# Kernel tuning notes

Hardware: AMD Instinct MI355X
Metric: run time of the kernel (lower is better)

Reference implementation:

```python
import jax, jax.numpy as jnp
import numpy as np

EMBED_DIM = 1024
NUM_HEADS = 16
HEAD_DIM = EMBED_DIM // NUM_HEADS


def setup_inputs() -> dict:
    key = jax.random.key(0)
    ks = jax.random.split(key, 5)
    T, B, E = 2048, 2, EMBED_DIM
    s = 1.0 / np.sqrt(E)
    return {
        "x": jax.random.normal(ks[0], (T, B, E), jnp.float32),
        "wq": jax.random.normal(ks[1], (E, E), jnp.float32) * s,
        "bq": jnp.zeros((E,), jnp.float32),
        "wk": jax.random.normal(ks[2], (E, E), jnp.float32) * s,
        "bk": jnp.zeros((E,), jnp.float32),
        "wv": jax.random.normal(ks[3], (E, E), jnp.float32) * s,
        "bv": jnp.zeros((E,), jnp.float32),
        "wo": jax.random.normal(ks[4], (E, E), jnp.float32) * s,
        "bo": jnp.zeros((E,), jnp.float32),
    }


def reference(x, wq, bq, wk, bk, wv, bv, wo, bo):
    # x: [T, B, E] (Time x Batch x Channel), self-attention: query = key = value = x
    T, B, E = x.shape
    H, D = NUM_HEADS, HEAD_DIM
    scaling = D ** -0.5
    # Linear projections (torch Linear: y = x @ W.T + b)
    q = (jnp.einsum('tbe,fe->tbf', x, wq) + bq) * scaling
    k = jnp.einsum('tbe,fe->tbf', x, wk) + bk
    v = jnp.einsum('tbe,fe->tbf', x, wv) + bv
    # reshape to [B*H, T, D] equivalent -> use [B, H, T, D]
    q = q.reshape(T, B, H, D).transpose(1, 2, 0, 3)  # [B,H,T,D]
    k = k.reshape(T, B, H, D).transpose(1, 2, 0, 3)
    v = v.reshape(T, B, H, D).transpose(1, 2, 0, 3)
    # scores: [B,H,T,S], fp32 softmax
    scores = jnp.einsum('bhtd,bhsd->bhts', q, k)
    probs = jax.nn.softmax(scores.astype(jnp.float32), axis=-1).astype(x.dtype)
    attn = jnp.einsum('bhts,bhsd->bhtd', probs, v)  # [B,H,T,D]
    attn = attn.transpose(2, 0, 1, 3).reshape(T, B, E)
    out = jnp.einsum('tbe,fe->tbf', attn, wo) + bo
    return out
```

## Files before the change

kernel.cpp:

```cpp
#include <hip/hip_runtime.h>
#include <cstddef>
#include <cstdint>

#define T_DIM 2048
#define E_DIM 1024
#define M_DIM 4096

typedef __attribute__((ext_vector_type(8))) short short8;
typedef __attribute__((ext_vector_type(8))) _Float16 half8;
typedef __attribute__((ext_vector_type(4))) _Float16 half4;
typedef __attribute__((ext_vector_type(4))) float f32x4;

__device__ __forceinline__ short f16_bits(float v) {
  return __builtin_bit_cast(short, (_Float16)v);
}
__device__ __forceinline__ unsigned int pk2(float a, float b) {
  return __builtin_bit_cast(unsigned int, __builtin_amdgcn_cvt_pkrtz(a, b));
}
__device__ __forceinline__ half8 h8(short8 s) { return __builtin_bit_cast(half8, s); }

__device__ __forceinline__ void gl_lds16(const short* g, const short* l) {
  __builtin_amdgcn_global_load_lds(
      (const __attribute__((address_space(1))) unsigned int*)g,
      (__attribute__((address_space(3))) unsigned int*)l, 16, 0, 0);
}

__global__ __launch_bounds__(256) void convert_all(
    const float* __restrict__ x, const float* __restrict__ wq,
    const float* __restrict__ wk, const float* __restrict__ wv,
    const float* __restrict__ wo,
    short* __restrict__ xh, short* __restrict__ wqh, short* __restrict__ wkh,
    short* __restrict__ wvh, short* __restrict__ woh)
{
  const int bid = blockIdx.x;
  const float* in; short* hi; int base;
  if (bid < 4096)      { in = x;  hi = xh;  base = 0;    }
  else if (bid < 5120) { in = wq; hi = wqh; base = 4096; }
  else if (bid < 6144) { in = wk; hi = wkh; base = 5120; }
  else if (bid < 7168) { in = wv; hi = wvh; base = 6144; }
  else                 { in = wo; hi = woh; base = 7168; }
  const int i = (bid - base) * 256 + threadIdx.x;
  float4 v = ((const float4*)in)[i];
  uint2 p;
  p.x = (unsigned short)f16_bits(v.x) | ((unsigned int)(unsigned short)f16_bits(v.y) << 16);
  p.y = (unsigned short)f16_bits(v.z) | ((unsigned int)(unsigned short)f16_bits(v.w) << 16);
  ((uint2*)hi)[i] = p;
}

__global__ __launch_bounds__(256) void gemm_qkv(
    const short* __restrict__ xh,
    const short* __restrict__ wqh, const short* __restrict__ wkh,
    const short* __restrict__ wvh,
    const float* __restrict__ bq, const float* __restrict__ bk,
    const float* __restrict__ bv,
    short* __restrict__ qo, short* __restrict__ ko, short* __restrict__ vto)
{
  __shared__ __align__(16) short smem[128 * 64 * 2];
  short* Ah = smem;
  short* Wh = smem + 8192;
  const int tid = threadIdx.x;
  const int lane = tid & 63;
  const int w = tid >> 6;
  const int quad = lane >> 4;
  const int l15 = lane & 15;
  const int sel = blockIdx.x >> 3;
  const int n0 = (blockIdx.x & 7) * 128;
  const int m0 = blockIdx.y * 128;

  const short* wsel = sel == 0 ? wqh : sel == 1 ? wkh : wvh;
  const float* bias = sel == 0 ? bq : sel == 1 ? bk : bv;
  const float scale = sel == 0 ? 0.125f * 1.44269504088896f : 1.0f;

  const short* gsrc = (w < 2) ? xh : wsel;
  short* lbuf = (w < 2) ? Ah : Wh;
  const int rbase = (w < 2) ? m0 : n0;
  const int lrow8 = lane >> 3;
  const int gph8 = lane & 7;
  const int kg = (gph8 - lrow8) & 7;

  f32x4 zero = {0.f, 0.f, 0.f, 0.f};
  f32x4 acc[4][4];
#pragma unroll
  for (int i = 0; i < 4; ++i)
#pragma unroll
    for (int j = 0; j < 4; ++j) acc[i][j] = zero;

  const int wm = w & 1, wn = w >> 1;

  for (int k0 = 0; k0 < E_DIM; k0 += 64) {
    __syncthreads();
#pragma unroll
    for (int jj = 0; jj < 8; ++jj) {
      int j = (w & 1) * 8 + jj;
      int r = j * 8 + lrow8;
      gl_lds16(gsrc + (size_t)(rbase + r) * E_DIM + k0 + kg * 8, lbuf + j * 512);
    }
    __syncthreads();
#pragma unroll
    for (int ks = 0; ks < 2; ++ks) {
      short8 ahf[4];
#pragma unroll
      for (int i = 0; i < 4; ++i) {
        int r = wm * 64 + i * 16 + l15;
        ahf[i] = *(const short8*)&Ah[r * 64 + ((ks * 4 + quad + r) & 7) * 8];
      }
#pragma unroll
      for (int j = 0; j < 4; ++j) {
        int r = wn * 64 + j * 16 + l15;
        short8 bhf = *(const short8*)&Wh[r * 64 + ((ks * 4 + quad + r) & 7) * 8];
#pragma unroll
        for (int i = 0; i < 4; ++i)
          acc[i][j] = __builtin_amdgcn_mfma_f32_16x16x32_f16(h8(ahf[i]), h8(bhf), acc[i][j], 0, 0, 0);
      }
    }
  }

  if (sel < 2) {
#pragma unroll
    for (int j = 0; j < 4; ++j) {
      const int gc = n0 + wn * 64 + j * 16 + l15;
      const float bb = bias[gc];
      const int h = gc >> 6, d = gc & 63;
      short* dst = sel == 0 ? qo : ko;
#pragma unroll
      for (int i = 0; i < 4; ++i)
#pragma unroll
        for (int reg = 0; reg < 4; ++reg) {
          const int gm = m0 + wm * 64 + i * 16 + quad * 4 + reg;
          const float val = (acc[i][j][reg] + bb) * scale;
          const int t = gm >> 1, b = gm & 1;
          dst[((size_t)(b * 16 + h) * T_DIM + t) * 64 + d] = f16_bits(val);
        }
    }
  } else {
    short* Tb = smem;
    const int by = blockIdx.y;
#pragma unroll
    for (int R = 0; R < 2; ++R) {
      __syncthreads();
      if (wn == R) {
#pragma unroll
        for (int j = 0; j < 4; ++j) {
          const int nl = j * 16 + l15;
          const int gc = n0 + R * 64 + nl;
          const float bb = bias[gc];
#pragma unroll
          for (int i = 0; i < 4; ++i) {
            const int tp = wm * 32 + i * 8 + quad * 2;
            unsigned int lo = pk2(acc[i][j][0] + bb, acc[i][j][2] + bb);
            unsigned int hi = pk2(acc[i][j][1] + bb, acc[i][j][3] + bb);
            const int g0 = tp >> 3;
            const int sub = tp & 7;
            *(unsigned int*)&Tb[nl * 128 + ((g0 + nl) & 15) * 8 + sub] = lo;
            *(unsigned int*)&Tb[nl * 128 + ((g0 + 8 + nl) & 15) * 8 + sub] = hi;
          }
        }
      }
      __syncthreads();
#pragma unroll
      for (int ii = 0; ii < 4; ++ii) {
        const int n = w * 16 + ii * 4 + quad;
        const int g = (l15 - n) & 15;
        short8 vvec = *(const short8*)&Tb[n * 128 + l15 * 8];
        const int gc = n0 + R * 64 + n;
        const int h = gc >> 6, d = gc & 63;
        const int b = g >> 3;
        const int t = by * 64 + (g & 7) * 8;
        *(short8*)&vto[((size_t)(b * 16 + h) * 64 + d) * T_DIM + t] = vvec;
      }
    }
  }
}

__global__ __launch_bounds__(512, 4) void gemm_out_fused(
    const short* __restrict__ attn, const short* __restrict__ woh,
    const float* __restrict__ bo, float* __restrict__ out)
{
  __shared__ __align__(16) short smem[32768];
  const int tid = threadIdx.x;
  const int lane = tid & 63;
  const int w = tid >> 6;
  const int g = w >> 2;
  const int wg = w & 3;
  const int quad = lane >> 4;
  const int l15 = lane & 15;
  const int n0 = blockIdx.x * 128;
  const int m0 = blockIdx.y * 128;

  short* Ah = smem + g * 16384;
  short* Wh = Ah + 8192;
  const short* gsrc = (wg < 2) ? attn : woh;
  short* lbuf = (wg < 2) ? Ah : Wh;
  const int rbase = (wg < 2) ? m0 : n0;
  const int lrow8 = lane >> 3;
  const int gph8 = lane & 7;
  const int kg = (gph8 - lrow8) & 7;

  f32x4 zero = {0.f, 0.f, 0.f, 0.f};
  f32x4 acc[4][4];
#pragma unroll
  for (int i = 0; i < 4; ++i)
#pragma unroll
    for (int j = 0; j < 4; ++j) acc[i][j] = zero;

  const int wm = wg & 1, wn = wg >> 1;

  for (int k0 = g * 512; k0 < g * 512 + 512; k0 += 64) {
    __syncthreads();
#pragma unroll
    for (int jj = 0; jj < 8; ++jj) {
      int j = (wg & 1) * 8 + jj;
      int r = j * 8 + lrow8;
      gl_lds16(gsrc + (size_t)(rbase + r) * E_DIM + k0 + kg * 8, lbuf + j * 512);
    }
    __syncthreads();
#pragma unroll
    for (int ks = 0; ks < 2; ++ks) {
      short8 ahf[4];
#pragma unroll
      for (int i = 0; i < 4; ++i) {
        int r = wm * 64 + i * 16 + l15;
        ahf[i] = *(const short8*)&Ah[r * 64 + ((ks * 4 + quad + r) & 7) * 8];
      }
#pragma unroll
      for (int j = 0; j < 4; ++j) {
        int r = wn * 64 + j * 16 + l15;
        short8 bhf = *(const short8*)&Wh[r * 64 + ((ks * 4 + quad + r) & 7) * 8];
#pragma unroll
        for (int i = 0; i < 4; ++i)
          acc[i][j] = __builtin_amdgcn_mfma_f32_16x16x32_f16(h8(ahf[i]), h8(bhf), acc[i][j], 0, 0, 0);
      }
    }
  }

  __syncthreads();
  f32x4* Osc = (f32x4*)smem;
  if (g == 1) {
    f32x4* dst = Osc + wg * 1024;
#pragma unroll
    for (int i = 0; i < 4; ++i)
#pragma unroll
      for (int j = 0; j < 4; ++j)
        dst[(i * 4 + j) * 64 + lane] = acc[i][j];
  }
  __syncthreads();
  if (g == 0) {
    f32x4* src = Osc + wg * 1024;
#pragma unroll
    for (int j = 0; j < 4; ++j) {
      const int gc = n0 + wn * 64 + j * 16 + l15;
      const float bb = bo[gc];
#pragma unroll
      for (int i = 0; i < 4; ++i) {
        f32x4 t = src[(i * 4 + j) * 64 + lane];
#pragma unroll
        for (int reg = 0; reg < 4; ++reg) {
          const int gm = m0 + wm * 64 + i * 16 + quad * 4 + reg;
          out[(size_t)gm * E_DIM + gc] = acc[i][j][reg] + t[reg] + bb;
        }
      }
    }
  }
}

__global__ __launch_bounds__(256, 2) void attn_mfma(
    const short* __restrict__ q, const short* __restrict__ k,
    const short* __restrict__ vt, short* __restrict__ attn)
{
  __shared__ __align__(16) short SMEM[32768];
  __shared__ float l_red[4][128];
  short* Qs = SMEM;
  short* KV = SMEM + 8192;

  const int tid = threadIdx.x;
  const int lane = tid & 63;
  const int w = tid >> 6;
  const int quad = lane >> 4;
  const int l15 = lane & 15;

  const int fid = blockIdx.y * 16 + blockIdx.x;
  const int bhid = fid & 31;
  const int t0 = (fid >> 5) * 128;
  const int b = bhid >> 4, h = bhid & 15;

  const short* qb = q + (size_t)bhid * T_DIM * 64;
  const short* kb = k + (size_t)bhid * T_DIM * 64;
  const short* vb = vt + (size_t)bhid * 64 * T_DIM;

  const int lrow8 = lane >> 3;
  const int gph8 = lane & 7;

#pragma unroll
  for (int jj = 0; jj < 4; ++jj) {
    int j = w * 4 + jj;
    int r = j * 8 + lrow8;
    int gl = (gph8 - (r >> 1)) & 7;
    gl_lds16(qb + (size_t)(t0 + r) * 64 + gl * 8, Qs + j * 512);
  }

  const int kg = (gph8 - lrow8) & 7;
  const int vd = lane >> 1, vh = lane & 1;
#pragma unroll
  for (int c0 = 0; c0 < 2; ++c0) {
    short* slot = KV + c0 * 8192 + w * 2048;
    const int sg = c0 * 64 + w * 16;
    gl_lds16(kb + (size_t)(sg + lrow8) * 64 + kg * 8, slot);
    gl_lds16(kb + (size_t)(sg + lrow8 + 8) * 64 + kg * 8, slot + 512);
    gl_lds16(vb + (size_t)vd * T_DIM + sg + vh * 8, slot + 1024);
    gl_lds16(vb + (size_t)(vd + 32) * T_DIM + sg + vh * 8, slot + 1536);
  }
  __syncthreads();

  short8 qa[8][2];
#pragma unroll
  for (int qbk = 0; qbk < 8; ++qbk)
#pragma unroll
    for (int st = 0; st < 2; ++st) {
      int r = qbk * 16 + l15;
      int idx = r * 64 + (((st * 4 + quad) + (r >> 1)) & 7) * 8;
      qa[qbk][st] = *(const short8*)&Qs[idx];
    }

  f32x4 zero = {0.f, 0.f, 0.f, 0.f};
  f32x4 acc[4][8];
  float l_part[8];
#pragma unroll
  for (int d = 0; d < 4; ++d)
#pragma unroll
    for (int qb2 = 0; qb2 < 8; ++qb2) acc[d][qb2] = zero;
#pragma unroll
  for (int i = 0; i < 8; ++i) l_part[i] = 0.f;

  for (int c = 0; c < 32; ++c) {
    if (c >= 2) {
      if (c == 31) __builtin_amdgcn_s_waitcnt(0x0F70);
      else         __builtin_amdgcn_s_waitcnt(0x0F74);
    }
    const short* slot = KV + (c % 3) * 8192 + w * 2048;

    short8 kf[2];
#pragma unroll
    for (int st = 0; st < 2; ++st)
      kf[st] = *(const short8*)&slot[l15 * 64 + (((st * 4 + quad) + l15) & 7) * 8];
    uint2 vfu[4];
#pragma unroll
    for (int dblk = 0; dblk < 4; ++dblk)
      vfu[dblk] = *(const uint2*)&slot[1024 + (dblk * 16 + l15) * 16 + quad * 4];

    if (c < 30) {
      short* nslot = KV + ((c + 2) % 3) * 8192 + w * 2048;
      const int sg = (c + 2) * 64 + w * 16;
      gl_lds16(kb + (size_t)(sg + lrow8) * 64 + kg * 8, nslot);
      gl_lds16(kb + (size_t)(sg + lrow8 + 8) * 64 + kg * 8, nslot + 512);
      gl_lds16(vb + (size_t)vd * T_DIM + sg + vh * 8, nslot + 1024);
      gl_lds16(vb + (size_t)(vd + 32) * T_DIM + sg + vh * 8, nslot + 1536);
    }

    __builtin_amdgcn_s_setprio(1);
    uint2 pb[8];
#pragma unroll
    for (int qbk = 0; qbk < 8; ++qbk) {
      f32x4 s = zero;
      s = __builtin_amdgcn_mfma_f32_16x16x32_f16(h8(kf[0]), h8(qa[qbk][0]), s, 0, 0, 0);
      s = __builtin_amdgcn_mfma_f32_16x16x32_f16(h8(kf[1]), h8(qa[qbk][1]), s, 0, 0, 0);
      float p0 = __builtin_amdgcn_exp2f(s[0]);
      float p1 = __builtin_amdgcn_exp2f(s[1]);
      float p2 = __builtin_amdgcn_exp2f(s[2]);
      float p3 = __builtin_amdgcn_exp2f(s[3]);
      l_part[qbk] += (p0 + p1) + (p2 + p3);
      pb[qbk].x = pk2(p0, p1);
      pb[qbk].y = pk2(p2, p3);
    }

#pragma unroll
    for (int dblk = 0; dblk < 4; ++dblk) {
      half4 va = __builtin_bit_cast(half4, vfu[dblk]);
#pragma unroll
      for (int qbk = 0; qbk < 8; ++qbk)
        acc[dblk][qbk] = __builtin_amdgcn_mfma_f32_16x16x16f16(
            va, __builtin_bit_cast(half4, pb[qbk]), acc[dblk][qbk], 0, 0, 0);
    }
    __builtin_amdgcn_s_setprio(0);
  }

#pragma unroll
  for (int qbk = 0; qbk < 8; ++qbk) {
    float l = l_part[qbk];
    l += __shfl_xor(l, 16);
    l += __shfl_xor(l, 32);
    if (quad == 0) l_red[w][qbk * 16 + l15] = l;
  }

  f32x4* Osc = (f32x4*)SMEM;
  __syncthreads();
  if (w & 1) {
    f32x4* dst = Osc + (w >> 1) * 2048;
#pragma unroll
    for (int dblk = 0; dblk < 4; ++dblk)
#pragma unroll
      for (int qbk = 0; qbk < 8; ++qbk)
        dst[(dblk * 8 + qbk) * 64 + lane] = acc[dblk][qbk];
  }
  __syncthreads();
  if (!(w & 1)) {
    f32x4* src = Osc + (w >> 1) * 2048;
#pragma unroll
    for (int dblk = 0; dblk < 4; ++dblk)
#pragma unroll
      for (int qbk = 0; qbk < 8; ++qbk) {
        f32x4 t = src[(dblk * 8 + qbk) * 64 + lane];
        acc[dblk][qbk][0] += t[0]; acc[dblk][qbk][1] += t[1];
        acc[dblk][qbk][2] += t[2]; acc[dblk][qbk][3] += t[3];
      }
  }
  __syncthreads();
  if (w == 2) {
#pragma unroll
    for (int d2 = 0; d2 < 2; ++d2)
#pragma unroll
      for (int qbk = 0; qbk < 8; ++qbk)
        Osc[(d2 * 8 + qbk) * 64 + lane] = acc[d2][qbk];
  }
  if (w == 0) {
#pragma unroll
    for (int d2 = 0; d2 < 2; ++d2)
#pragma unroll
      for (int qbk = 0; qbk < 8; ++qbk)
        Osc[1024 + (d2 * 8 + qbk) * 64 + lane] = acc[2 + d2][qbk];
  }
  __syncthreads();
  if (w == 0) {
#pragma unroll
    for (int qbk = 0; qbk < 8; ++qbk) {
      const int qq = qbk * 16 + l15;
      const float lsum = l_red[0][qq] + l_red[1][qq] + l_red[2][qq] + l_red[3][qq];
      const float inv = 1.f / lsum;
      const int t = t0 + qq;
      const size_t mrow = (size_t)(t * 2 + b) * E_DIM;
#pragma unroll
      for (int d2 = 0; d2 < 2; ++d2) {
        f32x4 t4 = Osc[(d2 * 8 + qbk) * 64 + lane];
        uint2 ov;
        ov.x = pk2((acc[d2][qbk][0] + t4[0]) * inv, (acc[d2][qbk][1] + t4[1]) * inv);
        ov.y = pk2((acc[d2][qbk][2] + t4[2]) * inv, (acc[d2][qbk][3] + t4[3]) * inv);
        *(uint2*)&attn[mrow + h * 64 + d2 * 16 + quad * 4] = ov;
      }
    }
  }
  if (w == 2) {
#pragma unroll
    for (int qbk = 0; qbk < 8; ++qbk) {
      const int qq = qbk * 16 + l15;
      const float lsum = l_red[0][qq] + l_red[1][qq] + l_red[2][qq] + l_red[3][qq];
      const float inv = 1.f / lsum;
      const int t = t0 + qq;
      const size_t mrow = (size_t)(t * 2 + b) * E_DIM;
#pragma unroll
      for (int d2 = 0; d2 < 2; ++d2) {
        f32x4 t4 = Osc[1024 + (d2 * 8 + qbk) * 64 + lane];
        uint2 ov;
        ov.x = pk2((acc[2 + d2][qbk][0] + t4[0]) * inv, (acc[2 + d2][qbk][1] + t4[1]) * inv);
        ov.y = pk2((acc[2 + d2][qbk][2] + t4[2]) * inv, (acc[2 + d2][qbk][3] + t4[3]) * inv);
        *(uint2*)&attn[mrow + h * 64 + (2 + d2) * 16 + quad * 4] = ov;
      }
    }
  }
}

extern "C" void kernel_launch(void* const* d_in, const int* in_sizes, int n_in,
                              void* d_out, int out_size, void* d_ws, size_t ws_size,
                              hipStream_t stream)
{
  const float* x  = (const float*)d_in[0];
  const float* wq = (const float*)d_in[1];
  const float* bq = (const float*)d_in[2];
  const float* wk = (const float*)d_in[3];
  const float* bk = (const float*)d_in[4];
  const float* wv = (const float*)d_in[5];
  const float* bv = (const float*)d_in[6];
  const float* wo = (const float*)d_in[7];
  const float* bo = (const float*)d_in[8];
  float* out = (float*)d_out;

  short* ws = (short*)d_ws;
  const size_t M4 = (size_t)M_DIM * E_DIM;
  const size_t M1 = (size_t)E_DIM * E_DIM;
  short* aws  = ws;
  short* woh  = aws + M4;
  short* xh   = woh + M1;
  short* wqh  = xh + M4;
  short* wkh  = wqh + M1;
  short* wvh  = wkh + M1;
  short* qws  = wvh + M1;
  short* kws  = qws + M4;
  short* vtws = kws + M4;

  convert_all<<<8192, 256, 0, stream>>>(x, wq, wk, wv, wo, xh, wqh, wkh, wvh, woh);
  gemm_qkv<<<dim3(24, 32), 256, 0, stream>>>(xh, wqh, wkh, wvh, bq, bk, bv,
                                             qws, kws, vtws);
  attn_mfma<<<dim3(16, 32), 256, 0, stream>>>(qws, kws, vtws, aws);
  gemm_out_fused<<<dim3(8, 32), 512, 0, stream>>>(aws, woh, bo, out);
}
```

Baseline: 196.0 us.

## Store V row-major and use LDS transpose reads instead of GEMM-side transpose

The QKV projection epilogue no longer transposes V through shared memory into a [B,H,D,T] layout. It writes V in the same [B,H,T,D] layout as Q and K. The attention kernel now loads V rows directly and uses ds_read_b64_tr_b16 transposing LDS reads to build the MFMA operand. This removes the extra LDS round trip and syncs in the projection epilogue. In exchange it adds inline asm with explicit lgkmcnt waits and sched barriers, which may constrain instruction scheduling in the attention loop.

```diff
diff --git a/kernel.cpp b/kernel.cpp
--- a/kernel.cpp
+++ b/kernel.cpp
@@ -10,6 +10,7 @@
 typedef __attribute__((ext_vector_type(8))) _Float16 half8;
 typedef __attribute__((ext_vector_type(4))) _Float16 half4;
 typedef __attribute__((ext_vector_type(4))) float f32x4;
+typedef __attribute__((ext_vector_type(2))) unsigned int uint32x2;
 
 __device__ __forceinline__ short f16_bits(float v) {
   return __builtin_bit_cast(short, (_Float16)v);
@@ -115,60 +116,21 @@
     }
   }
 
-  if (sel < 2) {
-#pragma unroll
-    for (int j = 0; j < 4; ++j) {
-      const int gc = n0 + wn * 64 + j * 16 + l15;
-      const float bb = bias[gc];
-      const int h = gc >> 6, d = gc & 63;
-      short* dst = sel == 0 ? qo : ko;
-#pragma unroll
-      for (int i = 0; i < 4; ++i)
-#pragma unroll
-        for (int reg = 0; reg < 4; ++reg) {
-          const int gm = m0 + wm * 64 + i * 16 + quad * 4 + reg;
-          const float val = (acc[i][j][reg] + bb) * scale;
-          const int t = gm >> 1, b = gm & 1;
-          dst[((size_t)(b * 16 + h) * T_DIM + t) * 64 + d] = f16_bits(val);
-        }
-    }
-  } else {
-    short* Tb = smem;
-    const int by = blockIdx.y;
-#pragma unroll
-    for (int R = 0; R < 2; ++R) {
-      __syncthreads();
-      if (wn == R) {
-#pragma unroll
-        for (int j = 0; j < 4; ++j) {
-          const int nl = j * 16 + l15;
-          const int gc = n0 + R * 64 + nl;
-          const float bb = bias[gc];
-#pragma unroll
-          for (int i = 0; i < 4; ++i) {
-            const int tp = wm * 32 + i * 8 + quad * 2;
-            unsigned int lo = pk2(acc[i][j][0] + bb, acc[i][j][2] + bb);
-            unsigned int hi = pk2(acc[i][j][1] + bb, acc[i][j][3] + bb);
-            const int g0 = tp >> 3;
-            const int sub = tp & 7;
-            *(unsigned int*)&Tb[nl * 128 + ((g0 + nl) & 15) * 8 + sub] = lo;
-            *(unsigned int*)&Tb[nl * 128 + ((g0 + 8 + nl) & 15) * 8 + sub] = hi;
-          }
-        }
-      }
-      __syncthreads();
-#pragma unroll
-      for (int ii = 0; ii < 4; ++ii) {
-        const int n = w * 16 + ii * 4 + quad;
-        const int g = (l15 - n) & 15;
-        short8 vvec = *(const short8*)&Tb[n * 128 + l15 * 8];
-        const int gc = n0 + R * 64 + n;
-        const int h = gc >> 6, d = gc & 63;
-        const int b = g >> 3;
-        const int t = by * 64 + (g & 7) * 8;
-        *(short8*)&vto[((size_t)(b * 16 + h) * 64 + d) * T_DIM + t] = vvec;
-      }
-    }
+  short* dst = sel == 0 ? qo : sel == 1 ? ko : vto;
+#pragma unroll
+  for (int j = 0; j < 4; ++j) {
+    const int gc = n0 + wn * 64 + j * 16 + l15;
+    const float bb = bias[gc];
+    const int h = gc >> 6, d = gc & 63;
+#pragma unroll
+    for (int i = 0; i < 4; ++i)
+#pragma unroll
+      for (int reg = 0; reg < 4; ++reg) {
+        const int gm = m0 + wm * 64 + i * 16 + quad * 4 + reg;
+        const float val = (acc[i][j][reg] + bb) * scale;
+        const int t = gm >> 1, b = gm & 1;
+        dst[((size_t)(b * 16 + h) * T_DIM + t) * 64 + d] = f16_bits(val);
+      }
   }
 }
 
@@ -285,7 +247,7 @@
 
   const short* qb = q + (size_t)bhid * T_DIM * 64;
   const short* kb = k + (size_t)bhid * T_DIM * 64;
-  const short* vb = vt + (size_t)bhid * 64 * T_DIM;
+  const short* vb = vt + (size_t)bhid * T_DIM * 64;
 
   const int lrow8 = lane >> 3;
   const int gph8 = lane & 7;
@@ -298,16 +260,19 @@
     gl_lds16(qb + (size_t)(t0 + r) * 64 + gl * 8, Qs + j * 512);
   }
 
+  const int vs  = (lane >> 1) & 15;
+  const int vdd = lane >> 5;
+  const int vg2 = lane & 1;
+
   const int kg = (gph8 - lrow8) & 7;
-  const int vd = lane >> 1, vh = lane & 1;
 #pragma unroll
   for (int c0 = 0; c0 < 2; ++c0) {
     short* slot = KV + c0 * 8192 + w * 2048;
     const int sg = c0 * 64 + w * 16;
     gl_lds16(kb + (size_t)(sg + lrow8) * 64 + kg * 8, slot);
     gl_lds16(kb + (size_t)(sg + lrow8 + 8) * 64 + kg * 8, slot + 512);
-    gl_lds16(vb + (size_t)vd * T_DIM + sg + vh * 8, slot + 1024);
-    gl_lds16(vb + (size_t)(vd + 32) * T_DIM + sg + vh * 8, slot + 1536);
+    gl_lds16(vb + (size_t)(sg + vs) * 64 + vdd * 16 + vg2 * 8, slot + 1024);
+    gl_lds16(vb + (size_t)(sg + vs) * 64 + (2 + vdd) * 16 + vg2 * 8, slot + 1536);
   }
   __syncthreads();
 
@@ -335,25 +300,30 @@
     if (c >= 2) {
       if (c == 31) __builtin_amdgcn_s_waitcnt(0x0F70);
       else         __builtin_amdgcn_s_waitcnt(0x0F74);
+      __builtin_amdgcn_sched_barrier(0);
     }
     const short* slot = KV + (c % 3) * 8192 + w * 2048;
+
+    const __attribute__((address_space(3))) char* vaddr =
+        (const __attribute__((address_space(3))) char*)(slot + 1024) + lane * 8;
+    uint32x2 vf0, vf1, vf2, vf3;
+    asm volatile("ds_read_b64_tr_b16 %0, %1 offset:0"    : "=v"(vf0) : "v"(vaddr));
+    asm volatile("ds_read_b64_tr_b16 %0, %1 offset:512"  : "=v"(vf1) : "v"(vaddr));
+    asm volatile("ds_read_b64_tr_b16 %0, %1 offset:1024" : "=v"(vf2) : "v"(vaddr));
+    asm volatile("ds_read_b64_tr_b16 %0, %1 offset:1536" : "=v"(vf3) : "v"(vaddr));
 
     short8 kf[2];
 #pragma unroll
     for (int st = 0; st < 2; ++st)
       kf[st] = *(const short8*)&slot[l15 * 64 + (((st * 4 + quad) + l15) & 7) * 8];
-    uint2 vfu[4];
-#pragma unroll
-    for (int dblk = 0; dblk < 4; ++dblk)
-      vfu[dblk] = *(const uint2*)&slot[1024 + (dblk * 16 + l15) * 16 + quad * 4];
 
     if (c < 30) {
       short* nslot = KV + ((c + 2) % 3) * 8192 + w * 2048;
       const int sg = (c + 2) * 64 + w * 16;
       gl_lds16(kb + (size_t)(sg + lrow8) * 64 + kg * 8, nslot);
       gl_lds16(kb + (size_t)(sg + lrow8 + 8) * 64 + kg * 8, nslot + 512);
-      gl_lds16(vb + (size_t)vd * T_DIM + sg + vh * 8, nslot + 1024);
-      gl_lds16(vb + (size_t)(vd + 32) * T_DIM + sg + vh * 8, nslot + 1536);
+      gl_lds16(vb + (size_t)(sg + vs) * 64 + vdd * 16 + vg2 * 8, nslot + 1024);
+      gl_lds16(vb + (size_t)(sg + vs) * 64 + (2 + vdd) * 16 + vg2 * 8, nslot + 1536);
     }
 
     __builtin_amdgcn_s_setprio(1);
@@ -372,9 +342,13 @@
       pb[qbk].y = pk2(p2, p3);
     }
 
+    asm volatile("s_waitcnt lgkmcnt(0)" ::: "memory");
+    __builtin_amdgcn_sched_barrier(0);
+
 #pragma unroll
     for (int dblk = 0; dblk < 4; ++dblk) {
-      half4 va = __builtin_bit_cast(half4, vfu[dblk]);
+      uint32x2 vfu = dblk == 0 ? vf0 : dblk == 1 ? vf1 : dblk == 2 ? vf2 : vf3;
+      half4 va = __builtin_bit_cast(half4, vfu);
 #pragma unroll
       for (int qbk = 0; qbk < 8; ++qbk)
         acc[dblk][qbk] = __builtin_amdgcn_mfma_f32_16x16x16f16(
```

New measurement: 203.0 us. +3.5%, slower.

## Give each attention wave its own query rows, removing cross-wave output reduction

Applied to the files above, without the earlier changes.

The attention kernel no longer splits each key chunk across the four waves, which forced an LDS reduction of partial outputs and row sums at the end. Now each wave owns 16 query rows and walks all keys. Each block handles 64 queries instead of 128, so the launch grid doubles. A two-slot K/V double buffer with block barriers replaces the three-slot waitcnt pipeline, and LDS shrinks so launch bounds can request four blocks per CU. The trade-off is that each K/V tile is now loaded by twice as many blocks, and V fragments are re-read from LDS for every key sub-tile.

```diff
diff --git a/kernel.cpp b/kernel.cpp
--- a/kernel.cpp
+++ b/kernel.cpp
@@ -263,14 +263,12 @@
   }
 }
 
-__global__ __launch_bounds__(256, 2) void attn_mfma(
+__global__ __launch_bounds__(256, 4) void attn_mfma(
     const short* __restrict__ q, const short* __restrict__ k,
     const short* __restrict__ vt, short* __restrict__ attn)
 {
-  __shared__ __align__(16) short SMEM[32768];
-  __shared__ float l_red[4][128];
-  short* Qs = SMEM;
-  short* KV = SMEM + 8192;
+  __shared__ __align__(16) short SMEM[16384];
+  short* Qs = SMEM + 8192;
 
   const int tid = threadIdx.x;
   const int lane = tid & 63;
@@ -278,9 +276,9 @@
   const int quad = lane >> 4;
   const int l15 = lane & 15;
 
-  const int fid = blockIdx.y * 16 + blockIdx.x;
+  const int fid = blockIdx.y * 32 + blockIdx.x;
   const int bhid = fid & 31;
-  const int t0 = (fid >> 5) * 128;
+  const int t0 = (fid >> 5) * 64;
   const int b = bhid >> 4, h = bhid & 15;
 
   const short* qb = q + (size_t)bhid * T_DIM * 64;
@@ -289,181 +287,99 @@
 
   const int lrow8 = lane >> 3;
   const int gph8 = lane & 7;
-
-#pragma unroll
-  for (int jj = 0; jj < 4; ++jj) {
-    int j = w * 4 + jj;
+  const int kg = (gph8 - lrow8) & 7;
+
+#pragma unroll
+  for (int jj = 0; jj < 2; ++jj) {
+    int j = w * 2 + jj;
     int r = j * 8 + lrow8;
     int gl = (gph8 - (r >> 1)) & 7;
     gl_lds16(qb + (size_t)(t0 + r) * 64 + gl * 8, Qs + j * 512);
   }
-
-  const int kg = (gph8 - lrow8) & 7;
-  const int vd = lane >> 1, vh = lane & 1;
-#pragma unroll
-  for (int c0 = 0; c0 < 2; ++c0) {
-    short* slot = KV + c0 * 8192 + w * 2048;
-    const int sg = c0 * 64 + w * 16;
-    gl_lds16(kb + (size_t)(sg + lrow8) * 64 + kg * 8, slot);
-    gl_lds16(kb + (size_t)(sg + lrow8 + 8) * 64 + kg * 8, slot + 512);
-    gl_lds16(vb + (size_t)vd * T_DIM + sg + vh * 8, slot + 1024);
-    gl_lds16(vb + (size_t)(vd + 32) * T_DIM + sg + vh * 8, slot + 1536);
+#pragma unroll
+  for (int jj = 0; jj < 2; ++jj) {
+    const int row = w * 16 + jj * 8 + lrow8;
+    gl_lds16(kb + (size_t)row * 64 + kg * 8, SMEM + (w * 16 + jj * 8) * 64);
+    gl_lds16(vb + (size_t)row * T_DIM + kg * 8, SMEM + 4096 + (w * 16 + jj * 8) * 64);
   }
   __syncthreads();
 
-  short8 qa[8][2];
-#pragma unroll
-  for (int qbk = 0; qbk < 8; ++qbk)
-#pragma unroll
-    for (int st = 0; st < 2; ++st) {
-      int r = qbk * 16 + l15;
-      int idx = r * 64 + (((st * 4 + quad) + (r >> 1)) & 7) * 8;
-      qa[qbk][st] = *(const short8*)&Qs[idx];
-    }
-
-  f32x4 zero = {0.f, 0.f, 0.f, 0.f};
-  f32x4 acc[4][8];
-  float l_part[8];
-#pragma unroll
-  for (int d = 0; d < 4; ++d)
-#pragma unroll
-    for (int qb2 = 0; qb2 < 8; ++qb2) acc[d][qb2] = zero;
-#pragma unroll
-  for (int i = 0; i < 8; ++i) l_part[i] = 0.f;
+  short8 qa[2];
+  {
+    const int r = w * 16 + l15;
+#pragma unroll
+    for (int st = 0; st < 2; ++st)
+      qa[st] = *(const short8*)&Qs[r * 64 + ((st * 4 + quad + (r >> 1)) & 7) * 8];
+  }
+  __syncthreads();
+
+  const f32x4 zero = {0.f, 0.f, 0.f, 0.f};
+  f32x4 acc[4];
+#pragma unroll
+  for (int d = 0; d < 4; ++d) acc[d] = zero;
+  float lp = 0.f;
 
   for (int c = 0; c < 32; ++c) {
-    if (c >= 2) {
-      if (c == 31) __builtin_amdgcn_s_waitcnt(0x0F70);
-      else         __builtin_amdgcn_s_waitcnt(0x0F74);
-    }
-    const short* slot = KV + (c % 3) * 8192 + w * 2048;
-
-    short8 kf[2];
-#pragma unroll
-    for (int st = 0; st < 2; ++st)
-      kf[st] = *(const short8*)&slot[l15 * 64 + (((st * 4 + quad) + l15) & 7) * 8];
-    uint2 vfu[4];
-#pragma unroll
-    for (int dblk = 0; dblk < 4; ++dblk)
-      vfu[dblk] = *(const uint2*)&slot[1024 + (dblk * 16 + l15) * 16 + quad * 4];
-
-    if (c < 30) {
-      short* nslot = KV + ((c + 2) % 3) * 8192 + w * 2048;
-      const int sg = (c + 2) * 64 + w * 16;
-      gl_lds16(kb + (size_t)(sg + lrow8) * 64 + kg * 8, nslot);
-      gl_lds16(kb + (size_t)(sg + lrow8 + 8) * 64 + kg * 8, nslot + 512);
-      gl_lds16(vb + (size_t)vd * T_DIM + sg + vh * 8, nslot + 1024);
-      gl_lds16(vb + (size_t)(vd + 32) * T_DIM + sg + vh * 8, nslot + 1536);
-    }
+    if (c > 0) __syncthreads();
+    if (c < 31) {
+      short* ns = SMEM + ((c + 1) & 1) * 8192;
+#pragma unroll
+      for (int jj = 0; jj < 2; ++jj) {
+        const int row = w * 16 + jj * 8 + lrow8;
+        gl_lds16(kb + (size_t)((c + 1) * 64 + row) * 64 + kg * 8,
+                 ns + (w * 16 + jj * 8) * 64);
+        gl_lds16(vb + (size_t)row * T_DIM + (c + 1) * 64 + kg * 8,
+                 ns + 4096 + (w * 16 + jj * 8) * 64);
+      }
+    }
+    const short* slot = SMEM + (c & 1) * 8192;
 
     __builtin_amdgcn_s_setprio(1);
-    uint2 pb[8];
-#pragma unroll
-    for (int qbk = 0; qbk < 8; ++qbk) {
+    uint2 pb[4];
+#pragma unroll
+    for (int stile = 0; stile < 4; ++stile) {
+      const int kr = (stile * 16 + l15) * 64;
+      short8 kf0 = *(const short8*)&slot[kr + ((quad + l15) & 7) * 8];
+      short8 kf1 = *(const short8*)&slot[kr + ((4 + quad + l15) & 7) * 8];
       f32x4 s = zero;
-      s = __builtin_amdgcn_mfma_f32_16x16x32_f16(h8(kf[0]), h8(qa[qbk][0]), s, 0, 0, 0);
-      s = __builtin_amdgcn_mfma_f32_16x16x32_f16(h8(kf[1]), h8(qa[qbk][1]), s, 0, 0, 0);
+      s = __builtin_amdgcn_mfma_f32_16x16x32_f16(h8(kf0), h8(qa[0]), s, 0, 0, 0);
+      s = __builtin_amdgcn_mfma_f32_16x16x32_f16(h8(kf1), h8(qa[1]), s, 0, 0, 0);
       float p0 = __builtin_amdgcn_exp2f(s[0]);
       float p1 = __builtin_amdgcn_exp2f(s[1]);
       float p2 = __builtin_amdgcn_exp2f(s[2]);
       float p3 = __builtin_amdgcn_exp2f(s[3]);
-      l_part[qbk] += (p0 + p1) + (p2 + p3);
-      pb[qbk].x = pk2(p0, p1);
-      pb[qbk].y = pk2(p2, p3);
-    }
-
-#pragma unroll
-    for (int dblk = 0; dblk < 4; ++dblk) {
-      half4 va = __builtin_bit_cast(half4, vfu[dblk]);
-#pragma unroll
-      for (int qbk = 0; qbk < 8; ++qbk)
-        acc[dblk][qbk] = __builtin_amdgcn_mfma_f32_16x16x16f16(
-            va, __builtin_bit_cast(half4, pb[qbk]), acc[dblk][qbk], 0, 0, 0);
+      lp += (p0 + p1) + (p2 + p3);
+      pb[stile].x = pk2(p0, p1);
+      pb[stile].y = pk2(p2, p3);
+    }
+
+#pragma unroll
+    for (int stile = 0; stile < 4; ++stile) {
+      const int g = stile * 2 + (quad >> 1);
+#pragma unroll
+      for (int dblk = 0; dblk < 4; ++dblk) {
+        uint2 va = *(const uint2*)&slot[4096 + (dblk * 16 + l15) * 64 +
+                                        ((g + l15) & 7) * 8 + (quad & 1) * 4];
+        acc[dblk] = __builtin_amdgcn_mfma_f32_16x16x16f16(
+            __builtin_bit_cast(half4, va), __builtin_bit_cast(half4, pb[stile]),
+            acc[dblk], 0, 0, 0);
+      }
     }
     __builtin_amdgcn_s_setprio(0);
   }
 
-#pragma unroll
-  for (int qbk = 0; qbk < 8; ++qbk) {
-    float l = l_part[qbk];
-    l += __shfl_xor(l, 16);
-    l += __shfl_xor(l, 32);
-    if (quad == 0) l_red[w][qbk * 16 + l15] = l;
-  }
-
-  f32x4* Osc = (f32x4*)SMEM;
-  __syncthreads();
-  if (w & 1) {
-    f32x4* dst = Osc + (w >> 1) * 2048;
-#pragma unroll
-    for (int dblk = 0; dblk < 4; ++dblk)
-#pragma unroll
-      for (int qbk = 0; qbk < 8; ++qbk)
-        dst[(dblk * 8 + qbk) * 64 + lane] = acc[dblk][qbk];
-  }
-  __syncthreads();
-  if (!(w & 1)) {
-    f32x4* src = Osc + (w >> 1) * 2048;
-#pragma unroll
-    for (int dblk = 0; dblk < 4; ++dblk)
-#pragma unroll
-      for (int qbk = 0; qbk < 8; ++qbk) {
-        f32x4 t = src[(dblk * 8 + qbk) * 64 + lane];
-        acc[dblk][qbk][0] += t[0]; acc[dblk][qbk][1] += t[1];
-        acc[dblk][qbk][2] += t[2]; acc[dblk][qbk][3] += t[3];
-      }
-  }
-  __syncthreads();
-  if (w == 2) {
-#pragma unroll
-    for (int d2 = 0; d2 < 2; ++d2)
-#pragma unroll
-      for (int qbk = 0; qbk < 8; ++qbk)
-        Osc[(d2 * 8 + qbk) * 64 + lane] = acc[d2][qbk];
-  }
-  if (w == 0) {
-#pragma unroll
-    for (int d2 = 0; d2 < 2; ++d2)
-#pragma unroll
-      for (int qbk = 0; qbk < 8; ++qbk)
-        Osc[1024 + (d2 * 8 + qbk) * 64 + lane] = acc[2 + d2][qbk];
-  }
-  __syncthreads();
-  if (w == 0) {
-#pragma unroll
-    for (int qbk = 0; qbk < 8; ++qbk) {
-      const int qq = qbk * 16 + l15;
-      const float lsum = l_red[0][qq] + l_red[1][qq] + l_red[2][qq] + l_red[3][qq];
-      const float inv = 1.f / lsum;
-      const int t = t0 + qq;
-      const size_t mrow = (size_t)(t * 2 + b) * E_DIM;
-#pragma unroll
-      for (int d2 = 0; d2 < 2; ++d2) {
-        f32x4 t4 = Osc[(d2 * 8 + qbk) * 64 + lane];
-        uint2 ov;
-        ov.x = pk2((acc[d2][qbk][0] + t4[0]) * inv, (acc[d2][qbk][1] + t4[1]) * inv);
-        ov.y = pk2((acc[d2][qbk][2] + t4[2]) * inv, (acc[d2][qbk][3] + t4[3]) * inv);
-        *(uint2*)&attn[mrow + h * 64 + d2 * 16 + quad * 4] = ov;
-      }
-    }
-  }
-  if (w == 2) {
-#pragma unroll
-    for (int qbk = 0; qbk < 8; ++qbk) {
-      const int qq = qbk * 16 + l15;
-      const float lsum = l_red[0][qq] + l_red[1][qq] + l_red[2][qq] + l_red[3][qq];
-      const float inv = 1.f / lsum;
-      const int t = t0 + qq;
-      const size_t mrow = (size_t)(t * 2 + b) * E_DIM;
-#pragma unroll
-      for (int d2 = 0; d2 < 2; ++d2) {
-        f32x4 t4 = Osc[1024 + (d2 * 8 + qbk) * 64 + lane];
-        uint2 ov;
-        ov.x = pk2((acc[2 + d2][qbk][0] + t4[0]) * inv, (acc[2 + d2][qbk][1] + t4[1]) * inv);
-        ov.y = pk2((acc[2 + d2][qbk][2] + t4[2]) * inv, (acc[2 + d2][qbk][3] + t4[3]) * inv);
-        *(uint2*)&attn[mrow + h * 64 + (2 + d2) * 16 + quad * 4] = ov;
-      }
-    }
+  lp += __shfl_xor(lp, 16);
+  lp += __shfl_xor(lp, 32);
+  const float inv = 1.f / lp;
+
+  const int t = t0 + w * 16 + l15;
+  const size_t mrow = (size_t)(t * 2 + b) * E_DIM;
+#pragma unroll
+  for (int dblk = 0; dblk < 4; ++dblk) {
+    uint2 ov;
+    ov.x = pk2(acc[dblk][0] * inv, acc[dblk][1] * inv);
+    ov.y = pk2(acc[dblk][2] * inv, acc[dblk][3] * inv);
+    *(uint2*)&attn[mrow + h * 64 + dblk * 16 + quad * 4] = ov;
   }
 }
 
@@ -498,6 +414,6 @@
   convert_all<<<8192, 256, 0, stream>>>(x, wq, wk, wv, wo, xh, wqh, wkh, wvh, woh);
   gemm_qkv<<<dim3(24, 32), 256, 0, stream>>>(xh, wqh, wkh, wvh, bq, bk, bv,
                                              qws, kws, vtws);
-  attn_mfma<<<dim3(16, 32), 256, 0, stream>>>(qws, kws, vtws, aws);
+  attn_mfma<<<dim3(32, 32), 256, 0, stream>>>(qws, kws, vtws, aws);
   gemm_out_fused<<<dim3(8, 32), 512, 0, stream>>>(aws, woh, bo, out);
 }
```

New measurement: 205.1 us. +4.7%, slower.

## Halve attention query tile, use double buffering, raise occupancy and grid size

Applied to the files above, without the earlier changes.

The attention kernel now handles 64 query rows per block instead of 128, which doubles the grid to 1024 blocks. The K/V prefetch goes from a three-slot ring with two stages in flight to a two-slot ping-pong with one stage in flight. Q shares its LDS region with l_red, and launch bounds rise to 3 blocks per CU. The aim is better CU fill and more latency hiding through occupancy, at the cost of loading each K/V tile twice as often per query row and having less prefetch depth.

```diff
diff --git a/kernel.cpp b/kernel.cpp
--- a/kernel.cpp
+++ b/kernel.cpp
@@ -263,14 +263,14 @@
   }
 }
 
-__global__ __launch_bounds__(256, 2) void attn_mfma(
+__global__ __launch_bounds__(256, 3) void attn_mfma(
     const short* __restrict__ q, const short* __restrict__ k,
     const short* __restrict__ vt, short* __restrict__ attn)
 {
-  __shared__ __align__(16) short SMEM[32768];
-  __shared__ float l_red[4][128];
-  short* Qs = SMEM;
-  short* KV = SMEM + 8192;
+  __shared__ __align__(16) short SMEM[20480];
+  short* KV = SMEM;
+  short* Qs = SMEM + 16384;
+  float* l_red = (float*)(SMEM + 16384);
 
   const int tid = threadIdx.x;
   const int lane = tid & 63;
@@ -278,9 +278,9 @@
   const int quad = lane >> 4;
   const int l15 = lane & 15;
 
-  const int fid = blockIdx.y * 16 + blockIdx.x;
+  const int fid = blockIdx.y * 32 + blockIdx.x;
   const int bhid = fid & 31;
-  const int t0 = (fid >> 5) * 128;
+  const int t0 = (fid >> 5) * 64;
   const int b = bhid >> 4, h = bhid & 15;
 
   const short* qb = q + (size_t)bhid * T_DIM * 64;
@@ -289,21 +289,19 @@
 
   const int lrow8 = lane >> 3;
   const int gph8 = lane & 7;
-
-#pragma unroll
-  for (int jj = 0; jj < 4; ++jj) {
-    int j = w * 4 + jj;
+  const int kg = (gph8 - lrow8) & 7;
+  const int vd = lane >> 1, vh = lane & 1;
+
+#pragma unroll
+  for (int jj = 0; jj < 2; ++jj) {
+    int j = w * 2 + jj;
     int r = j * 8 + lrow8;
     int gl = (gph8 - (r >> 1)) & 7;
     gl_lds16(qb + (size_t)(t0 + r) * 64 + gl * 8, Qs + j * 512);
   }
-
-  const int kg = (gph8 - lrow8) & 7;
-  const int vd = lane >> 1, vh = lane & 1;
-#pragma unroll
-  for (int c0 = 0; c0 < 2; ++c0) {
-    short* slot = KV + c0 * 8192 + w * 2048;
-    const int sg = c0 * 64 + w * 16;
+  {
+    short* slot = KV + w * 2048;
+    const int sg = w * 16;
     gl_lds16(kb + (size_t)(sg + lrow8) * 64 + kg * 8, slot);
     gl_lds16(kb + (size_t)(sg + lrow8 + 8) * 64 + kg * 8, slot + 512);
     gl_lds16(vb + (size_t)vd * T_DIM + sg + vh * 8, slot + 1024);
@@ -311,32 +309,30 @@
   }
   __syncthreads();
 
-  short8 qa[8][2];
-#pragma unroll
-  for (int qbk = 0; qbk < 8; ++qbk)
+  short8 qa[4][2];
+#pragma unroll
+  for (int qbk = 0; qbk < 4; ++qbk)
 #pragma unroll
     for (int st = 0; st < 2; ++st) {
       int r = qbk * 16 + l15;
       int idx = r * 64 + (((st * 4 + quad) + (r >> 1)) & 7) * 8;
       qa[qbk][st] = *(const short8*)&Qs[idx];
     }
-
-  f32x4 zero = {0.f, 0.f, 0.f, 0.f};
-  f32x4 acc[4][8];
-  float l_part[8];
+  __syncthreads();
+
+  const f32x4 zero = {0.f, 0.f, 0.f, 0.f};
+  f32x4 acc[4][4];
+  float l_part[4];
 #pragma unroll
   for (int d = 0; d < 4; ++d)
 #pragma unroll
-    for (int qb2 = 0; qb2 < 8; ++qb2) acc[d][qb2] = zero;
-#pragma unroll
-  for (int i = 0; i < 8; ++i) l_part[i] = 0.f;
+    for (int qb2 = 0; qb2 < 4; ++qb2) acc[d][qb2] = zero;
+#pragma unroll
+  for (int i = 0; i < 4; ++i) l_part[i] = 0.f;
 
   for (int c = 0; c < 32; ++c) {
-    if (c >= 2) {
-      if (c == 31) __builtin_amdgcn_s_waitcnt(0x0F70);
-      else         __builtin_amdgcn_s_waitcnt(0x0F74);
-    }
-    const short* slot = KV + (c % 3) * 8192 + w * 2048;
+    if (c > 0) __builtin_amdgcn_s_waitcnt(0x0F70);
+    const short* slot = KV + (c & 1) * 8192 + w * 2048;
 
     short8 kf[2];
 #pragma unroll
@@ -347,9 +343,9 @@
     for (int dblk = 0; dblk < 4; ++dblk)
       vfu[dblk] = *(const uint2*)&slot[1024 + (dblk * 16 + l15) * 16 + quad * 4];
 
-    if (c < 30) {
-      short* nslot = KV + ((c + 2) % 3) * 8192 + w * 2048;
-      const int sg = (c + 2) * 64 + w * 16;
+    if (c < 31) {
+      short* nslot = KV + ((c + 1) & 1) * 8192 + w * 2048;
+      const int sg = (c + 1) * 64 + w * 16;
       gl_lds16(kb + (size_t)(sg + lrow8) * 64 + kg * 8, nslot);
       gl_lds16(kb + (size_t)(sg + lrow8 + 8) * 64 + kg * 8, nslot + 512);
       gl_lds16(vb + (size_t)vd * T_DIM + sg + vh * 8, nslot + 1024);
@@ -357,9 +353,9 @@
     }
 
     __builtin_amdgcn_s_setprio(1);
-    uint2 pb[8];
-#pragma unroll
-    for (int qbk = 0; qbk < 8; ++qbk) {
+    uint2 pb[4];
+#pragma unroll
+    for (int qbk = 0; qbk < 4; ++qbk) {
       f32x4 s = zero;
       s = __builtin_amdgcn_mfma_f32_16x16x32_f16(h8(kf[0]), h8(qa[qbk][0]), s, 0, 0, 0);
       s = __builtin_amdgcn_mfma_f32_16x16x32_f16(h8(kf[1]), h8(qa[qbk][1]), s, 0, 0, 0);
@@ -376,7 +372,7 @@
     for (int dblk = 0; dblk < 4; ++dblk) {
       half4 va = __builtin_bit_cast(half4, vfu[dblk]);
 #pragma unroll
-      for (int qbk = 0; qbk < 8; ++qbk)
+      for (int qbk = 0; qbk < 4; ++qbk)
         acc[dblk][qbk] = __builtin_amdgcn_mfma_f32_16x16x16f16(
             va, __builtin_bit_cast(half4, pb[qbk]), acc[dblk][qbk], 0, 0, 0);
     }
@@ -384,31 +380,31 @@
   }
 
 #pragma unroll
-  for (int qbk = 0; qbk < 8; ++qbk) {
+  for (int qbk = 0; qbk < 4; ++qbk) {
     float l = l_part[qbk];
     l += __shfl_xor(l, 16);
     l += __shfl_xor(l, 32);
-    if (quad == 0) l_red[w][qbk * 16 + l15] = l;
+    if (quad == 0) l_red[w * 64 + qbk * 16 + l15] = l;
   }
 
   f32x4* Osc = (f32x4*)SMEM;
   __syncthreads();
   if (w & 1) {
-    f32x4* dst = Osc + (w >> 1) * 2048;
+    f32x4* dst = Osc + (w >> 1) * 1024;
 #pragma unroll
     for (int dblk = 0; dblk < 4; ++dblk)
 #pragma unroll
-      for (int qbk = 0; qbk < 8; ++qbk)
-        dst[(dblk * 8 + qbk) * 64 + lane] = acc[dblk][qbk];
+      for (int qbk = 0; qbk < 4; ++qbk)
+        dst[(dblk * 4 + qbk) * 64 + lane] = acc[dblk][qbk];
   }
   __syncthreads();
   if (!(w & 1)) {
-    f32x4* src = Osc + (w >> 1) * 2048;
+    f32x4* src = Osc + (w >> 1) * 1024;
 #pragma unroll
     for (int dblk = 0; dblk < 4; ++dblk)
 #pragma unroll
-      for (int qbk = 0; qbk < 8; ++qbk) {
-        f32x4 t = src[(dblk * 8 + qbk) * 64 + lane];
+      for (int qbk = 0; qbk < 4; ++qbk) {
+        f32x4 t = src[(dblk * 4 + qbk) * 64 + lane];
         acc[dblk][qbk][0] += t[0]; acc[dblk][qbk][1] += t[1];
         acc[dblk][qbk][2] += t[2]; acc[dblk][qbk][3] += t[3];
       }
@@ -418,28 +414,29 @@
 #pragma unroll
     for (int d2 = 0; d2 < 2; ++d2)
 #pragma unroll
-      for (int qbk = 0; qbk < 8; ++qbk)
-        Osc[(d2 * 8 + qbk) * 64 + lane] = acc[d2][qbk];
+      for (int qbk = 0; qbk < 4; ++qbk)
+        Osc[(d2 * 4 + qbk) * 64 + lane] = acc[d2][qbk];
   }
   if (w == 0) {
 #pragma unroll
     for (int d2 = 0; d2 < 2; ++d2)
 #pragma unroll
-      for (int qbk = 0; qbk < 8; ++qbk)
-        Osc[1024 + (d2 * 8 + qbk) * 64 + lane] = acc[2 + d2][qbk];
+      for (int qbk = 0; qbk < 4; ++qbk)
+        Osc[512 + (d2 * 4 + qbk) * 64 + lane] = acc[2 + d2][qbk];
   }
   __syncthreads();
   if (w == 0) {
 #pragma unroll
-    for (int qbk = 0; qbk < 8; ++qbk) {
+    for (int qbk = 0; qbk < 4; ++qbk) {
       const int qq = qbk * 16 + l15;
-      const float lsum = l_red[0][qq] + l_red[1][qq] + l_red[2][qq] + l_red[3][qq];
+      const float lsum = l_red[0 * 64 + qq] + l_red[1 * 64 + qq] +
+                         l_red[2 * 64 + qq] + l_red[3 * 64 + qq];
       const float inv = 1.f / lsum;
       const int t = t0 + qq;
       const size_t mrow = (size_t)(t * 2 + b) * E_DIM;
 #pragma unroll
       for (int d2 = 0; d2 < 2; ++d2) {
-        f32x4 t4 = Osc[(d2 * 8 + qbk) * 64 + lane];
+        f32x4 t4 = Osc[(d2 * 4 + qbk) * 64 + lane];
         uint2 ov;
         ov.x = pk2((acc[d2][qbk][0] + t4[0]) * inv, (acc[d2][qbk][1] + t4[1]) * inv);
         ov.y = pk2((acc[d2][qbk][2] + t4[2]) * inv, (acc[d2][qbk][3] + t4[3]) * inv);
@@ -449,15 +446,16 @@
   }
   if (w == 2) {
 #pragma unroll
-    for (int qbk = 0; qbk < 8; ++qbk) {
+    for (int qbk = 0; qbk < 4; ++qbk) {
       const int qq = qbk * 16 + l15;
-      const float lsum = l_red[0][qq] + l_red[1][qq] + l_red[2][qq] + l_red[3][qq];
+      const float lsum = l_red[0 * 64 + qq] + l_red[1 * 64 + qq] +
+                         l_red[2 * 64 + qq] + l_red[3 * 64 + qq];
       const float inv = 1.f / lsum;
       const int t = t0 + qq;
       const size_t mrow = (size_t)(t * 2 + b) * E_DIM;
 #pragma unroll
       for (int d2 = 0; d2 < 2; ++d2) {
-        f32x4 t4 = Osc[1024 + (d2 * 8 + qbk) * 64 + lane];
+        f32x4 t4 = Osc[512 + (d2 * 4 + qbk) * 64 + lane];
         uint2 ov;
         ov.x = pk2((acc[2 + d2][qbk][0] + t4[0]) * inv, (acc[2 + d2][qbk][1] + t4[1]) * inv);
         ov.y = pk2((acc[2 + d2][qbk][2] + t4[2]) * inv, (acc[2 + d2][qbk][3] + t4[3]) * inv);
@@ -498,6 +496,6 @@
   convert_all<<<8192, 256, 0, stream>>>(x, wq, wk, wv, wo, xh, wqh, wkh, wvh, woh);
   gemm_qkv<<<dim3(24, 32), 256, 0, stream>>>(xh, wqh, wkh, wvh, bq, bk, bv,
                                              qws, kws, vtws);
-  attn_mfma<<<dim3(16, 32), 256, 0, stream>>>(qws, kws, vtws, aws);
+  attn_mfma<<<dim3(32, 32), 256, 0, stream>>>(qws, kws, vtws, aws);
   gemm_out_fused<<<dim3(8, 32), 512, 0, stream>>>(aws, woh, bo, out);
 }
```

Result: slower. 204.1 us (+4.1%).
